# Optimization experiments

Hardware: AMD Instinct MI355X
Metric: run time of the kernel (lower is better)

The kernel has to match this reference:

```python
import jax, jax.numpy as jnp
import numpy as np

B, S, D1, D2, NH, DFF, K, L = 16, 512, 512, 256, 8, 1024, 8192, 3
DK = D2 // NH
EPS_LN = 1e-5


def layer_norm(x, g, b):
    m = jnp.mean(x, axis=-1, keepdims=True)
    v = jnp.mean((x - m) ** 2, axis=-1, keepdims=True)
    return (x - m) * jax.lax.rsqrt(v + EPS_LN) * g + b


def setup_inputs() -> dict:
    key = jax.random.key(0)
    ks = jax.random.split(key, 16)
    w = lambda k, sh: (jax.random.normal(k, sh, dtype=jnp.float32) * 0.02)
    inp = {
        'x': jax.random.normal(ks[0], (B, S, D1), dtype=jnp.float32),
        'w_in': w(ks[1], (D1, D2)), 'b_in': jnp.zeros((D2,), jnp.float32),
        # per-layer stacked transformer params, leading dim = L
        'wq': w(ks[2], (L, D2, D2)), 'bq': jnp.zeros((L, D2), jnp.float32),
        'wk': w(ks[3], (L, D2, D2)), 'bk': jnp.zeros((L, D2), jnp.float32),
        'wv': w(ks[4], (L, D2, D2)), 'bv': jnp.zeros((L, D2), jnp.float32),
        'wo': w(ks[5], (L, D2, D2)), 'bo': jnp.zeros((L, D2), jnp.float32),
        'ln1_g': jnp.ones((L, D2), jnp.float32), 'ln1_b': jnp.zeros((L, D2), jnp.float32),
        'ln2_g': jnp.ones((L, D2), jnp.float32), 'ln2_b': jnp.zeros((L, D2), jnp.float32),
        'ff1_w': w(ks[6], (L, D2, DFF)), 'ff1_b': jnp.zeros((L, DFF), jnp.float32),
        'ff2_w': w(ks[7], (L, DFF, D2)), 'ff2_b': jnp.zeros((L, D2), jnp.float32),
        'pre_g': jnp.ones((D2,), jnp.float32), 'pre_b': jnp.zeros((D2,), jnp.float32),
        # codebook ~ U(-1/K, 1/K) as in torch init
        'codebook': jax.random.uniform(ks[8], (K, D2), jnp.float32, -1.0 / K, 1.0 / K),
    }
    return inp


def _encoder(x, w_in, b_in, wq, bq, wk, bk, wv, bv, wo, bo,
             ln1_g, ln1_b, ln2_g, ln2_b, ff1_w, ff1_b, ff2_w, ff2_b,
             pre_g, pre_b, codebook):
    h = x @ w_in + b_in  # [B,S,D2]
    scale = 1.0 / jnp.sqrt(jnp.float32(DK))
    for i in range(L):
        q = (h @ wq[i] + bq[i]).reshape(B, S, NH, DK)
        k = (h @ wk[i] + bk[i]).reshape(B, S, NH, DK)
        v = (h @ wv[i] + bv[i]).reshape(B, S, NH, DK)
        scores = jnp.einsum('bqhd,bkhd->bhqk', q, k) * scale
        attn = jax.nn.softmax(scores, axis=-1)  # dropout = identity (eval)
        ctx = jnp.einsum('bhqk,bkhd->bqhd', attn, v).reshape(B, S, D2)
        h = layer_norm(h + (ctx @ wo[i] + bo[i]), ln1_g[i], ln1_b[i])
        ff = jax.nn.gelu(h @ ff1_w[i] + ff1_b[i], approximate=False) @ ff2_w[i] + ff2_b[i]
        h = layer_norm(h + ff, ln2_g[i], ln2_b[i])
    h = layer_norm(h, pre_g, pre_b)

    # --- Vector quantization (L2 branch) ---
    flat = h.reshape(-1, D2)  # [N, D2], N = B*S
    dists = (jnp.sum(flat ** 2, axis=1, keepdims=True)
             + jnp.sum(codebook ** 2, axis=1)
             - 2.0 * flat @ codebook.T)  # [N, K]
    idx = jnp.argmin(dists, axis=1)  # [N]
    quant = codebook[idx].reshape(B, S, D2)  # gather == one-hot matmul
    sg = jax.lax.stop_gradient
    e_loss = jnp.mean((sg(quant) - h) ** 2)
    q_loss = jnp.mean((quant - sg(h)) ** 2)
    loss = q_loss + 0.25 * e_loss
    quant_st = h + sg(quant - h)  # straight-through
    n = jnp.float32(flat.shape[0])
    avg_probs = jnp.zeros((K,), jnp.float32).at[idx].add(1.0) / n
    perplexity = jnp.exp(-jnp.sum(avg_probs * jnp.log(avg_probs + 1e-10)))
    return quant_st, loss, perplexity, idx.reshape(B, S)


def reference(x, w_in, b_in, wq, bq, wk, bk, wv, bv, wo, bo,
              ln1_g, ln1_b, ln2_g, ln2_b, ff1_w, ff1_b, ff2_w, ff2_b,
              pre_g, pre_b, codebook):
    return _encoder(x, w_in, b_in, wq, bq, wk, bk, wv, bv, wo, bo,
                    ln1_g, ln1_b, ln2_g, ln2_b, ff1_w, ff1_b, ff2_w, ff2_b,
                    pre_g, pre_b, codebook)
```

## Files before the change

### kernel.cpp

```cpp
#include <hip/hip_runtime.h>
#include <cfloat>
#include <math.h>


#define NTOK 8192

__device__ __forceinline__ float np_pairwise256(const float* xs, int lane) {
  float r = 0.f;
  if (lane < 16) {
    const int b = lane >> 3, j = lane & 7;
    const float* p = xs + b * 128 + j;
    r = p[0];
#pragma unroll
    for (int i = 1; i < 16; i++) r += p[i * 8];
  }
  float r0 = __shfl(r, 0), r1 = __shfl(r, 1), r2 = __shfl(r, 2), r3 = __shfl(r, 3);
  float r4 = __shfl(r, 4), r5 = __shfl(r, 5), r6 = __shfl(r, 6), r7 = __shfl(r, 7);
  float s0 = ((r0 + r1) + (r2 + r3)) + ((r4 + r5) + (r6 + r7));
  float q0 = __shfl(r, 8), q1 = __shfl(r, 9), q2 = __shfl(r, 10), q3 = __shfl(r, 11);
  float q4 = __shfl(r, 12), q5 = __shfl(r, 13), q6 = __shfl(r, 14), q7 = __shfl(r, 15);
  float s1 = ((q0 + q1) + (q2 + q3)) + ((q4 + q5) + (q6 + q7));
  return s0 + s1;
}

__device__ __forceinline__ float gelu_np(float x) {
  const float SQRT2F = 1.4142135623730951f;
  float xs = x / SQRT2F;
  float e = (float)erf((double)xs);
  float t = 1.0f + e;
  return (0.5f * x) * t;
}

__device__ __forceinline__ void gemm128_core(
    const float* __restrict__ A, int lda, const float* __restrict__ Bw,
    const float* __restrict__ bias, float* __restrict__ C,
    int N, int klen, int act, int m0, int n0)
{
  __shared__ float As[16][132];
  __shared__ float Bs[16][132];
  const int tid = threadIdx.x;
  const int tx = tid & 15, ty = tid >> 4;
  const int ar = tid >> 1;
  const int ak = (tid & 1) * 8;
  const int brr = tid >> 5;
  const int bnn = (tid & 31) * 4;
  float accb[8][8] = {};
  const float* Ap = A + (m0 + ar) * lda + ak;
  const float* Bp = Bw + brr * N + n0 + bnn;

  for (int k0 = 0; k0 < klen; k0 += 16) {
    float4 a0 = *(const float4*)(Ap);
    float4 a1 = *(const float4*)(Ap + 4);
    float4 b0 = *(const float4*)(Bp);
    float4 b1 = *(const float4*)(Bp + 8 * N);
    As[ak + 0][ar] = a0.x; As[ak + 1][ar] = a0.y;
    As[ak + 2][ar] = a0.z; As[ak + 3][ar] = a0.w;
    As[ak + 4][ar] = a1.x; As[ak + 5][ar] = a1.y;
    As[ak + 6][ar] = a1.z; As[ak + 7][ar] = a1.w;
    *(float4*)&Bs[brr][bnn] = b0;
    *(float4*)&Bs[brr + 8][bnn] = b1;
    __syncthreads();
#pragma unroll
    for (int kk = 0; kk < 16; kk++) {
      float4 av0 = *(const float4*)&As[kk][ty * 8];
      float4 av1 = *(const float4*)&As[kk][ty * 8 + 4];
      float4 bv0 = *(const float4*)&Bs[kk][tx * 4];
      float4 bv1 = *(const float4*)&Bs[kk][64 + tx * 4];
      float a[8] = {av0.x, av0.y, av0.z, av0.w, av1.x, av1.y, av1.z, av1.w};
      float b[8] = {bv0.x, bv0.y, bv0.z, bv0.w, bv1.x, bv1.y, bv1.z, bv1.w};
#pragma unroll
      for (int i = 0; i < 8; i++)
#pragma unroll
        for (int j = 0; j < 8; j++) accb[i][j] = fmaf(a[i], b[j], accb[i][j]);
    }
    __syncthreads();
    Ap += 16;
    Bp += 16 * N;
  }
  float4 bbl = make_float4(0.f, 0.f, 0.f, 0.f);
  float4 bbh = make_float4(0.f, 0.f, 0.f, 0.f);
  if (bias) {
    bbl = *(const float4*)&bias[n0 + tx * 4];
    bbh = *(const float4*)&bias[n0 + 64 + tx * 4];
  }
#pragma unroll
  for (int i = 0; i < 8; i++) {
    const int m = m0 + ty * 8 + i;
    float4 lo, hi;
    lo.x = accb[i][0] + bbl.x; lo.y = accb[i][1] + bbl.y;
    lo.z = accb[i][2] + bbl.z; lo.w = accb[i][3] + bbl.w;
    hi.x = accb[i][4] + bbh.x; hi.y = accb[i][5] + bbh.y;
    hi.z = accb[i][6] + bbh.z; hi.w = accb[i][7] + bbh.w;
    if (act == 1) {
      lo.x = gelu_np(lo.x); lo.y = gelu_np(lo.y);
      lo.z = gelu_np(lo.z); lo.w = gelu_np(lo.w);
      hi.x = gelu_np(hi.x); hi.y = gelu_np(hi.y);
      hi.z = gelu_np(hi.z); hi.w = gelu_np(hi.w);
    }
    *(float4*)&C[m * N + n0 + tx * 4] = lo;
    *(float4*)&C[m * N + n0 + 64 + tx * 4] = hi;
  }
}

__global__ __launch_bounds__(256) void qkv_kernel(
    const float* __restrict__ h,
    const float* __restrict__ wq, const float* __restrict__ bq,
    const float* __restrict__ wk, const float* __restrict__ bk,
    const float* __restrict__ wv, const float* __restrict__ bv,
    float* __restrict__ Q, float* __restrict__ K, float* __restrict__ V)
{
  const int sel = blockIdx.y >> 1;
  const int n0 = (blockIdx.y & 1) * 128;
  const float* W = (sel == 0) ? wq : (sel == 1) ? wk : wv;
  const float* bb = (sel == 0) ? bq : (sel == 1) ? bk : bv;
  float* C = (sel == 0) ? Q : (sel == 1) ? K : V;
  gemm128_core(h, 256, W, bb, C, 256, 256, 0, blockIdx.x * 128, n0);
}

__global__ __launch_bounds__(256) void gemm128_kernel(
    const float* __restrict__ A, const float* __restrict__ B,
    const float* __restrict__ bias, float* __restrict__ C,
    int N, int K, int act)
{
  gemm128_core(A, K, B, bias, C, N, K, act, blockIdx.x * 128, blockIdx.y * 128);
}

__global__ __launch_bounds__(256) void gemm64_kernel(
    const float* __restrict__ A, const float* __restrict__ B,
    const float* __restrict__ bias, float* __restrict__ C,
    int M, int N, int K, int act)
{
  __shared__ float As[2][16][68];
  __shared__ float Bs[2][16][68];
  const int tid = threadIdx.x;
  const int tx = tid & 15, ty = tid >> 4;
  const int m0 = blockIdx.x * 64, n0 = blockIdx.y * 64;
  const int ar = tid >> 2;
  const int ak = (tid & 3) * 4;
  const int br = tid >> 4;
  const int bn = (tid & 15) * 4;
  const float* Ap = A + (m0 + ar) * K + ak;
  const float* Bp = B + br * N + n0 + bn;
  float acc[4][4] = {};
  float accb[4][4] = {};
  const int nk = K >> 4;

  float4 aR = *(const float4*)(Ap);
  float4 bR = *(const float4*)(Bp);
  As[0][ak + 0][ar] = aR.x; As[0][ak + 1][ar] = aR.y;
  As[0][ak + 2][ar] = aR.z; As[0][ak + 3][ar] = aR.w;
  *(float4*)&Bs[0][br][bn] = bR;

  for (int t = 0; t < nk; t++) {
    const int p = t & 1;
    __syncthreads();
    if (t + 1 < nk) {
      aR = *(const float4*)(Ap + (t + 1) * 16);
      bR = *(const float4*)(Bp + (t + 1) * 16 * N);
    }
#pragma unroll
    for (int kk = 0; kk < 16; kk++) {
      float4 av = *(const float4*)&As[p][kk][ty * 4];
      float4 bv = *(const float4*)&Bs[p][kk][tx * 4];
      float a[4] = {av.x, av.y, av.z, av.w};
      float b[4] = {bv.x, bv.y, bv.z, bv.w};
#pragma unroll
      for (int i = 0; i < 4; i++)
#pragma unroll
        for (int j = 0; j < 4; j++) accb[i][j] = fmaf(a[i], b[j], accb[i][j]);
    }
    if (((((t + 1) << 4) % 384) == 0) || (t + 1 == nk)) {
#pragma unroll
      for (int i = 0; i < 4; i++)
#pragma unroll
        for (int j = 0; j < 4; j++) { acc[i][j] += accb[i][j]; accb[i][j] = 0.f; }
    }
    if (t + 1 < nk) {
      const int q = p ^ 1;
      As[q][ak + 0][ar] = aR.x; As[q][ak + 1][ar] = aR.y;
      As[q][ak + 2][ar] = aR.z; As[q][ak + 3][ar] = aR.w;
      *(float4*)&Bs[q][br][bn] = bR;
    }
  }
  float4 bb4 = make_float4(0.f, 0.f, 0.f, 0.f);
  if (bias) bb4 = *(const float4*)&bias[n0 + tx * 4];
#pragma unroll
  for (int i = 0; i < 4; i++) {
    float4 o;
    o.x = acc[i][0] + bb4.x;
    o.y = acc[i][1] + bb4.y;
    o.z = acc[i][2] + bb4.z;
    o.w = acc[i][3] + bb4.w;
    if (act == 1) {
      o.x = gelu_np(o.x); o.y = gelu_np(o.y);
      o.z = gelu_np(o.z); o.w = gelu_np(o.w);
    }
    *(float4*)&C[(m0 + ty * 4 + i) * N + n0 + tx * 4] = o;
  }
}

__global__ __launch_bounds__(256) void attn_kernel(
    const float* __restrict__ Q, const float* __restrict__ Kb,
    const float* __restrict__ Vb, float* __restrict__ ctx)
{
  __shared__ float Qs[64][36];
  __shared__ float Ks[2][32][36];
  __shared__ float Vs[2][32][36];
  __shared__ float Ps[64][33];
  __shared__ float l_lds[64];
  const int tid = threadIdx.x;
  const int b = blockIdx.x >> 3, h = blockIdx.x & 7;
  const int q0 = blockIdx.y * 64;
  const int base = (b * 512) * 256 + h * 32;
  const float scale = 0.17677669529663687f;

  {
    int i0 = tid * 2;
    int r = i0 >> 3, c = i0 & 7;
    *(float4*)&Qs[r][c * 4] = *(const float4*)(Q + base + (q0 + r) * 256 + c * 4);
    int i1 = i0 + 1;
    r = i1 >> 3; c = i1 & 7;
    *(float4*)&Qs[r][c * 4] = *(const float4*)(Q + base + (q0 + r) * 256 + c * 4);
  }
  if (tid < 64) l_lds[tid] = 0.f;

  const int sr = tid >> 3, sc = tid & 7;
  {
    float4 k0v = *(const float4*)(Kb + base + sr * 256 + sc * 4);
    float4 v0v = *(const float4*)(Vb + base + sr * 256 + sc * 4);
    *(float4*)&Ks[0][sr][sc * 4] = k0v;
    *(float4*)&Vs[0][sr][sc * 4] = v0v;
  }

  const int tx = tid & 15, ty = tid >> 4;
  const int tx2 = tid & 7, ty2 = tid >> 3;
  float acc[2][4] = {};

  for (int kc = 0; kc < 16; kc++) {
    const int p = kc & 1;
    __syncthreads();
    float4 kst, vst;
    if (kc < 15) {
      int tok = (kc + 1) * 32 + sr;
      kst = *(const float4*)(Kb + base + tok * 256 + sc * 4);
      vst = *(const float4*)(Vb + base + tok * 256 + sc * 4);
    }
    float s0[4] = {}, s1[4] = {};
#pragma unroll
    for (int d = 0; d < 32; d += 4) {
      float4 k0 = *(const float4*)&Ks[p][tx][d];
      float4 k1 = *(const float4*)&Ks[p][tx + 16][d];
#pragma unroll
      for (int i = 0; i < 4; i++) {
        float4 qv = *(const float4*)&Qs[ty * 4 + i][d];
        s0[i] = fmaf(qv.w, k0.w, fmaf(qv.z, k0.z, fmaf(qv.y, k0.y, fmaf(qv.x, k0.x, s0[i]))));
        s1[i] = fmaf(qv.w, k1.w, fmaf(qv.z, k1.z, fmaf(qv.y, k1.y, fmaf(qv.x, k1.x, s1[i]))));
      }
    }
    if (kc < 15) {
      *(float4*)&Ks[p ^ 1][sr][sc * 4] = kst;
      *(float4*)&Vs[p ^ 1][sr][sc * 4] = vst;
    }
    float rs[4];
#pragma unroll
    for (int i = 0; i < 4; i++) {
      float p0 = expf(s0[i] * scale);
      float p1 = expf(s1[i] * scale);
      Ps[ty * 4 + i][tx] = p0;
      Ps[ty * 4 + i][tx + 16] = p1;
      rs[i] = p0 + p1;
    }
#pragma unroll
    for (int off = 1; off < 16; off <<= 1)
#pragma unroll
      for (int i = 0; i < 4; i++) rs[i] += __shfl_xor(rs[i], off);
    if (tx == 0) {
#pragma unroll
      for (int i = 0; i < 4; i++) l_lds[ty * 4 + i] += rs[i];
    }
    __syncthreads();
#pragma unroll 4
    for (int k = 0; k < 32; k++) {
      float4 vv = *(const float4*)&Vs[p][k][tx2 * 4];
      float pa = Ps[ty2 * 2][k];
      float pb = Ps[ty2 * 2 + 1][k];
      acc[0][0] = fmaf(pa, vv.x, acc[0][0]);
      acc[0][1] = fmaf(pa, vv.y, acc[0][1]);
      acc[0][2] = fmaf(pa, vv.z, acc[0][2]);
      acc[0][3] = fmaf(pa, vv.w, acc[0][3]);
      acc[1][0] = fmaf(pb, vv.x, acc[1][0]);
      acc[1][1] = fmaf(pb, vv.y, acc[1][1]);
      acc[1][2] = fmaf(pb, vv.z, acc[1][2]);
      acc[1][3] = fmaf(pb, vv.w, acc[1][3]);
    }
  }
  __syncthreads();
#pragma unroll
  for (int i = 0; i < 2; i++) {
    float inv = 1.f / l_lds[ty2 * 2 + i];
    float4 o;
    o.x = acc[i][0] * inv; o.y = acc[i][1] * inv;
    o.z = acc[i][2] * inv; o.w = acc[i][3] * inv;
    *(float4*)(ctx + base + (q0 + ty2 * 2 + i) * 256 + tx2 * 4) = o;
  }
}

__global__ __launch_bounds__(256) void ln_kernel(
    const float* __restrict__ X, const float* __restrict__ R,
    const float* __restrict__ g, const float* __restrict__ bt,
    float* __restrict__ Y, int hasR, float* __restrict__ Atok,
    int* __restrict__ counts, float* __restrict__ lossAcc)
{
  __shared__ float rows[4][256];
  const int w = threadIdx.x >> 6, lane = threadIdx.x & 63;
  float4 gv = *(const float4*)(g + lane * 4);
  float4 bv = *(const float4*)(bt + lane * 4);
  if (counts && blockIdx.x < 32) {
    int i = blockIdx.x * 256 + threadIdx.x;
    counts[i] = 0;
    if (i == 0) lossAcc[0] = 0.f;
  }
#pragma unroll 1
  for (int rr = 0; rr < 4; rr++) {
    const int row = blockIdx.x * 16 + w * 4 + rr;
    float4 xv = *(const float4*)(X + row * 256 + lane * 4);
    if (hasR) {
      float4 rv = *(const float4*)(R + row * 256 + lane * 4);
      xv.x += rv.x; xv.y += rv.y; xv.z += rv.z; xv.w += rv.w;
    }
    *(float4*)&rows[w][lane * 4] = xv;
    __syncthreads();
    float sum = np_pairwise256(rows[w], lane);
    float mean = sum * (1.0f / 256.0f);
    float dx = xv.x - mean, dy = xv.y - mean, dz = xv.z - mean, dw = xv.w - mean;
    __syncthreads();
    float4 sq; sq.x = dx * dx; sq.y = dy * dy; sq.z = dz * dz; sq.w = dw * dw;
    *(float4*)&rows[w][lane * 4] = sq;
    __syncthreads();
    float vsum = np_pairwise256(rows[w], lane);
    float var = vsum * (1.0f / 256.0f);
    float inv = 1.0f / sqrtf(var + 1e-5f);
    float4 o;
    o.x = ((dx * inv) * gv.x) + bv.x;
    o.y = ((dy * inv) * gv.y) + bv.y;
    o.z = ((dz * inv) * gv.z) + bv.z;
    o.w = ((dw * inv) * gv.w) + bv.w;
    *(float4*)(Y + row * 256 + lane * 4) = o;
    if (Atok) {
      float4 s2; s2.x = o.x * o.x; s2.y = o.y * o.y;
      s2.z = o.z * o.z; s2.w = o.w * o.w;
      __syncthreads();
      *(float4*)&rows[w][lane * 4] = s2;
      __syncthreads();
      float asum = np_pairwise256(rows[w], lane);
      if (lane == 0) Atok[row] = asum;
    }
    __syncthreads();
  }
}

__global__ __launch_bounds__(256) void vq_partial_kernel(
    const float* __restrict__ H, const float* __restrict__ CB,
    const float* __restrict__ Atok, float* __restrict__ partV,
    int* __restrict__ partI)
{
  __shared__ float As[16][132];
  __shared__ float Bs[16][132];
  const int tid = threadIdx.x;
  const int tx = tid & 15, ty = tid >> 4;
  const int m0 = blockIdx.x * 128;
  const int cg0 = blockIdx.y * 256;
  const int ar = tid >> 1;
  const int ak = (tid & 1) * 8;
  float At[8];
#pragma unroll
  for (int i = 0; i < 8; i++) At[i] = Atok[m0 + ty * 8 + i];
  float bestV[8];
  int bestI[8];
#pragma unroll
  for (int i = 0; i < 8; i++) { bestV[i] = FLT_MAX; bestI[i] = 0; }

  for (int ct = 0; ct < 2; ct++) {
    const int c0 = cg0 + ct * 128;
    float acc[8][8] = {};
    const float* Ap = H + (m0 + ar) * 256 + ak;
    const float* Bp = CB + (c0 + ar) * 256 + ak;
    for (int k0 = 0; k0 < 256; k0 += 16) {
      float4 a0 = *(const float4*)(Ap);
      float4 a1 = *(const float4*)(Ap + 4);
      float4 c0v = *(const float4*)(Bp);
      float4 c1v = *(const float4*)(Bp + 4);
      As[ak + 0][ar] = a0.x; As[ak + 1][ar] = a0.y;
      As[ak + 2][ar] = a0.z; As[ak + 3][ar] = a0.w;
      As[ak + 4][ar] = a1.x; As[ak + 5][ar] = a1.y;
      As[ak + 6][ar] = a1.z; As[ak + 7][ar] = a1.w;
      Bs[ak + 0][ar] = c0v.x; Bs[ak + 1][ar] = c0v.y;
      Bs[ak + 2][ar] = c0v.z; Bs[ak + 3][ar] = c0v.w;
      Bs[ak + 4][ar] = c1v.x; Bs[ak + 5][ar] = c1v.y;
      Bs[ak + 6][ar] = c1v.z; Bs[ak + 7][ar] = c1v.w;
      __syncthreads();
#pragma unroll
      for (int kk = 0; kk < 16; kk++) {
        float4 av0 = *(const float4*)&As[kk][ty * 8];
        float4 av1 = *(const float4*)&As[kk][ty * 8 + 4];
        float4 bv0 = *(const float4*)&Bs[kk][tx * 4];
        float4 bv1 = *(const float4*)&Bs[kk][64 + tx * 4];
        float a[8] = {av0.x, av0.y, av0.z, av0.w, av1.x, av1.y, av1.z, av1.w};
        float b[8] = {bv0.x, bv0.y, bv0.z, bv0.w, bv1.x, bv1.y, bv1.z, bv1.w};
#pragma unroll
        for (int i = 0; i < 8; i++)
#pragma unroll
          for (int j = 0; j < 8; j++) acc[i][j] = fmaf(a[i], b[j], acc[i][j]);
      }
      __syncthreads();
      Ap += 16;
      Bp += 16;
    }
#pragma unroll
    for (int i = 0; i < 8; i++) {
#pragma unroll
      for (int j = 0; j < 8; j++) {
        int code = c0 + ((j < 4) ? (tx * 4 + j) : (64 + tx * 4 + (j - 4)));
        float v = At[i] - 2.0f * acc[i][j];
        if (v < bestV[i]) { bestV[i] = v; bestI[i] = code; }
      }
    }
  }
#pragma unroll
  for (int i = 0; i < 8; i++) {
    float v = bestV[i];
    int ii = bestI[i];
#pragma unroll
    for (int off = 1; off < 16; off <<= 1) {
      float ov = __shfl_xor(v, off);
      int oi = __shfl_xor(ii, off);
      if (ov < v || (ov == v && oi < ii)) { v = ov; ii = oi; }
    }
    if (tx == 0) {
      int token = m0 + ty * 8 + i;
      partV[token * 32 + blockIdx.y] = v;
      partI[token * 32 + blockIdx.y] = ii;
    }
  }
}

__global__ __launch_bounds__(256) void vq_final_kernel(
    const float* __restrict__ partV, const int* __restrict__ partI,
    const float* __restrict__ HN, const float* __restrict__ CB,
    float* __restrict__ outQuant, float* __restrict__ outIdxF,
    int* __restrict__ idxInt, int* __restrict__ counts,
    float* __restrict__ lossAcc)
{
  const int w = threadIdx.x >> 6, lane = threadIdx.x & 63;
  const int t = blockIdx.x * 4 + w;
  float v = (lane < 32) ? partV[t * 32 + lane] : FLT_MAX;
  int i = (lane < 32) ? partI[t * 32 + lane] : 0x7fffffff;
#pragma unroll
  for (int off = 16; off; off >>= 1) {
    float ov = __shfl_xor(v, off);
    int oi = __shfl_xor(i, off);
    if (ov < v || (ov == v && oi < i)) { v = ov; i = oi; }
  }
  int idx = __shfl(i, 0);
  const float* c = CB + idx * 256;
  const float* hh = HN + t * 256;
  float4 cv = *(const float4*)(c + lane * 4);
  float4 hv = *(const float4*)(hh + lane * 4);
  *(float4*)(outQuant + t * 256 + lane * 4) = cv;
  float ex = cv.x - hv.x, ey = cv.y - hv.y, ez = cv.z - hv.z, ew = cv.w - hv.w;
  float se = ex * ex + ey * ey + ez * ez + ew * ew;
#pragma unroll
  for (int off = 32; off; off >>= 1) se += __shfl_xor(se, off);
  if (lane == 0) {
    outIdxF[t] = (float)idx;
    idxInt[t] = idx;
    atomicAdd(&counts[idx], 1);
    atomicAdd(lossAcc, se);
  }
}

__global__ __launch_bounds__(256) void vq_stats_kernel(
    const int* __restrict__ counts, const float* __restrict__ lossAcc,
    float* __restrict__ out)
{
  float ent = 0.f;
  for (int k = threadIdx.x; k < 8192; k += 256) {
    float p = (float)counts[k] * (1.0f / 8192.0f);
    ent += p * logf(p + 1e-10f);
  }
#pragma unroll
  for (int off = 32; off; off >>= 1) ent += __shfl_xor(ent, off);
  __shared__ float ws4[4];
  const int w = threadIdx.x >> 6, lane = threadIdx.x & 63;
  if (lane == 0) ws4[w] = ent;
  __syncthreads();
  if (threadIdx.x == 0) {
    float e = ws4[0] + ws4[1] + ws4[2] + ws4[3];
    out[2097152] = 1.25f * lossAcc[0] * (1.0f / 2097152.0f);
    out[2097153] = expf(-e);
  }
}

extern "C" void kernel_launch(void* const* d_in, const int* in_sizes, int n_in,
                              void* d_out, int out_size, void* d_ws, size_t ws_size,
                              hipStream_t stream) {
  const float* x = (const float*)d_in[0];
  const float* w_in = (const float*)d_in[1];
  const float* b_in = (const float*)d_in[2];
  const float* wq = (const float*)d_in[3];
  const float* bq = (const float*)d_in[4];
  const float* wk = (const float*)d_in[5];
  const float* bk = (const float*)d_in[6];
  const float* wv = (const float*)d_in[7];
  const float* bv = (const float*)d_in[8];
  const float* wo = (const float*)d_in[9];
  const float* bo = (const float*)d_in[10];
  const float* ln1g = (const float*)d_in[11];
  const float* ln1b = (const float*)d_in[12];
  const float* ln2g = (const float*)d_in[13];
  const float* ln2b = (const float*)d_in[14];
  const float* ff1w = (const float*)d_in[15];
  const float* ff1b = (const float*)d_in[16];
  const float* ff2w = (const float*)d_in[17];
  const float* ff2b = (const float*)d_in[18];
  const float* preg = (const float*)d_in[19];
  const float* preb = (const float*)d_in[20];
  const float* cb = (const float*)d_in[21];
  float* out = (float*)d_out;

  if (ws_size < (51ull << 20)) return;
  char* ws = (char*)d_ws;
  float* h = (float*)(ws + 0);
  float* Qb = (float*)(ws + (8ull << 20));
  float* Kb2 = (float*)(ws + (16ull << 20));
  float* Vb = (float*)(ws + (24ull << 20));
  float* Cx = (float*)(ws + (32ull << 20));
  float* Ob = Qb;
  float* F1 = Kb2;
  float* F2 = Qb;
  float* HN = Qb;
  char* smallbase = ws + (48ull << 20);
  float* Atok = (float*)(smallbase);
  float* partV = (float*)(smallbase + (512ull << 10));
  int* partI = (int*)(smallbase + (512ull << 10) + (1ull << 20));
  int* idxInt = (int*)(smallbase + (512ull << 10) + (2ull << 20));
  int* counts = (int*)(smallbase + (512ull << 10) + (2ull << 20) + (64ull << 10));
  float* lossAcc = (float*)(smallbase + (512ull << 10) + (2ull << 20) + (128ull << 10));

  gemm64_kernel<<<dim3(128, 4), 256, 0, stream>>>(x, w_in, b_in, h, NTOK, 256, 512, 0);

  for (int i = 0; i < 3; i++) {
    qkv_kernel<<<dim3(64, 6), 256, 0, stream>>>(
        h, wq + i * 65536, bq + i * 256, wk + i * 65536, bk + i * 256,
        wv + i * 65536, bv + i * 256, Qb, Kb2, Vb);
    attn_kernel<<<dim3(128, 8), 256, 0, stream>>>(Qb, Kb2, Vb, Cx);
    gemm64_kernel<<<dim3(128, 4), 256, 0, stream>>>(Cx, wo + i * 65536, bo + i * 256, Ob, NTOK, 256, 256, 0);
    ln_kernel<<<512, 256, 0, stream>>>(h, Ob, ln1g + i * 256, ln1b + i * 256, h, 1, nullptr, nullptr, nullptr);
    gemm128_kernel<<<dim3(64, 8), 256, 0, stream>>>(h, ff1w + i * 262144, ff1b + i * 1024, F1, 1024, 256, 1);
    gemm64_kernel<<<dim3(128, 4), 256, 0, stream>>>(F1, ff2w + i * 262144, ff2b + i * 256, F2, NTOK, 256, 1024, 0);
    ln_kernel<<<512, 256, 0, stream>>>(h, F2, ln2g + i * 256, ln2b + i * 256, h, 1, nullptr, nullptr, nullptr);
  }
  ln_kernel<<<512, 256, 0, stream>>>(h, nullptr, preg, preb, HN, 0, Atok, counts, lossAcc);

  vq_partial_kernel<<<dim3(64, 32), 256, 0, stream>>>(HN, cb, Atok, partV, partI);
  vq_final_kernel<<<2048, 256, 0, stream>>>(partV, partI, HN, cb,
                                            out, out + 2097154, idxInt, counts, lossAcc);
  vq_stats_kernel<<<1, 256, 0, stream>>>(counts, lossAcc, out);
}
```

Baseline: 1.533 ms.

## Drop attention K/V double buffering, flatten LayerNorm to one row per wave, add zero kernel

The attention kernel stops double-buffering K/V tiles. Each chunk is now loaded synchronously into a single LDS buffer, with an extra barrier before compute. The LayerNorm kernel handles one row per wave with 2048 blocks instead of looping over four rows, aiming for more parallelism. The counts and loss zeroing move into a separate small kernel. The attention change gives up load/compute overlap for less LDS use and simpler code, and the extra launch adds overhead.

```diff
diff --git a/kernel.cpp b/kernel.cpp
--- a/kernel.cpp
+++ b/kernel.cpp
@@ -204,8 +204,8 @@
     const float* __restrict__ Vb, float* __restrict__ ctx)
 {
   __shared__ float Qs[64][36];
-  __shared__ float Ks[2][32][36];
-  __shared__ float Vs[2][32][36];
+  __shared__ float Ks[32][36];
+  __shared__ float Vs[32][36];
   __shared__ float Ps[64][33];
   __shared__ float l_lds[64];
   const int tid = threadIdx.x;
@@ -224,42 +224,30 @@
   }
   if (tid < 64) l_lds[tid] = 0.f;
 
-  const int sr = tid >> 3, sc = tid & 7;
-  {
-    float4 k0v = *(const float4*)(Kb + base + sr * 256 + sc * 4);
-    float4 v0v = *(const float4*)(Vb + base + sr * 256 + sc * 4);
-    *(float4*)&Ks[0][sr][sc * 4] = k0v;
-    *(float4*)&Vs[0][sr][sc * 4] = v0v;
-  }
-
   const int tx = tid & 15, ty = tid >> 4;
   const int tx2 = tid & 7, ty2 = tid >> 3;
   float acc[2][4] = {};
 
   for (int kc = 0; kc < 16; kc++) {
-    const int p = kc & 1;
-    __syncthreads();
-    float4 kst, vst;
-    if (kc < 15) {
-      int tok = (kc + 1) * 32 + sr;
-      kst = *(const float4*)(Kb + base + tok * 256 + sc * 4);
-      vst = *(const float4*)(Vb + base + tok * 256 + sc * 4);
-    }
+    __syncthreads();
+    {
+      int r = tid >> 3, c = tid & 7;
+      int tok = kc * 32 + r;
+      *(float4*)&Ks[r][c * 4] = *(const float4*)(Kb + base + tok * 256 + c * 4);
+      *(float4*)&Vs[r][c * 4] = *(const float4*)(Vb + base + tok * 256 + c * 4);
+    }
+    __syncthreads();
     float s0[4] = {}, s1[4] = {};
 #pragma unroll
     for (int d = 0; d < 32; d += 4) {
-      float4 k0 = *(const float4*)&Ks[p][tx][d];
-      float4 k1 = *(const float4*)&Ks[p][tx + 16][d];
+      float4 k0 = *(const float4*)&Ks[tx][d];
+      float4 k1 = *(const float4*)&Ks[tx + 16][d];
 #pragma unroll
       for (int i = 0; i < 4; i++) {
         float4 qv = *(const float4*)&Qs[ty * 4 + i][d];
         s0[i] = fmaf(qv.w, k0.w, fmaf(qv.z, k0.z, fmaf(qv.y, k0.y, fmaf(qv.x, k0.x, s0[i]))));
         s1[i] = fmaf(qv.w, k1.w, fmaf(qv.z, k1.z, fmaf(qv.y, k1.y, fmaf(qv.x, k1.x, s1[i]))));
       }
-    }
-    if (kc < 15) {
-      *(float4*)&Ks[p ^ 1][sr][sc * 4] = kst;
-      *(float4*)&Vs[p ^ 1][sr][sc * 4] = vst;
     }
     float rs[4];
 #pragma unroll
@@ -281,7 +269,7 @@
     __syncthreads();
 #pragma unroll 4
     for (int k = 0; k < 32; k++) {
-      float4 vv = *(const float4*)&Vs[p][k][tx2 * 4];
+      float4 vv = *(const float4*)&Vs[k][tx2 * 4];
       float pa = Ps[ty2 * 2][k];
       float pb = Ps[ty2 * 2 + 1][k];
       acc[0][0] = fmaf(pa, vv.x, acc[0][0]);
@@ -308,54 +296,44 @@
 __global__ __launch_bounds__(256) void ln_kernel(
     const float* __restrict__ X, const float* __restrict__ R,
     const float* __restrict__ g, const float* __restrict__ bt,
-    float* __restrict__ Y, int hasR, float* __restrict__ Atok,
-    int* __restrict__ counts, float* __restrict__ lossAcc)
+    float* __restrict__ Y, int hasR, float* __restrict__ Atok)
 {
   __shared__ float rows[4][256];
   const int w = threadIdx.x >> 6, lane = threadIdx.x & 63;
+  const int row = blockIdx.x * 4 + w;
+  float4 xv = *(const float4*)(X + row * 256 + lane * 4);
+  if (hasR) {
+    float4 rv = *(const float4*)(R + row * 256 + lane * 4);
+    xv.x += rv.x; xv.y += rv.y; xv.z += rv.z; xv.w += rv.w;
+  }
+  *(float4*)&rows[w][lane * 4] = xv;
+  __syncthreads();
+  float sum = np_pairwise256(rows[w], lane);
+  float mean = sum * (1.0f / 256.0f);
+  float dx = xv.x - mean, dy = xv.y - mean, dz = xv.z - mean, dw = xv.w - mean;
+  __syncthreads();
+  float4 sq; sq.x = dx * dx; sq.y = dy * dy; sq.z = dz * dz; sq.w = dw * dw;
+  *(float4*)&rows[w][lane * 4] = sq;
+  __syncthreads();
+  float vsum = np_pairwise256(rows[w], lane);
+  float var = vsum * (1.0f / 256.0f);
+  float inv = 1.0f / sqrtf(var + 1e-5f);
   float4 gv = *(const float4*)(g + lane * 4);
   float4 bv = *(const float4*)(bt + lane * 4);
-  if (counts && blockIdx.x < 32) {
-    int i = blockIdx.x * 256 + threadIdx.x;
-    counts[i] = 0;
-    if (i == 0) lossAcc[0] = 0.f;
-  }
-#pragma unroll 1
-  for (int rr = 0; rr < 4; rr++) {
-    const int row = blockIdx.x * 16 + w * 4 + rr;
-    float4 xv = *(const float4*)(X + row * 256 + lane * 4);
-    if (hasR) {
-      float4 rv = *(const float4*)(R + row * 256 + lane * 4);
-      xv.x += rv.x; xv.y += rv.y; xv.z += rv.z; xv.w += rv.w;
-    }
-    *(float4*)&rows[w][lane * 4] = xv;
-    __syncthreads();
-    float sum = np_pairwise256(rows[w], lane);
-    float mean = sum * (1.0f / 256.0f);
-    float dx = xv.x - mean, dy = xv.y - mean, dz = xv.z - mean, dw = xv.w - mean;
-    __syncthreads();
-    float4 sq; sq.x = dx * dx; sq.y = dy * dy; sq.z = dz * dz; sq.w = dw * dw;
-    *(float4*)&rows[w][lane * 4] = sq;
-    __syncthreads();
-    float vsum = np_pairwise256(rows[w], lane);
-    float var = vsum * (1.0f / 256.0f);
-    float inv = 1.0f / sqrtf(var + 1e-5f);
-    float4 o;
-    o.x = ((dx * inv) * gv.x) + bv.x;
-    o.y = ((dy * inv) * gv.y) + bv.y;
-    o.z = ((dz * inv) * gv.z) + bv.z;
-    o.w = ((dw * inv) * gv.w) + bv.w;
-    *(float4*)(Y + row * 256 + lane * 4) = o;
-    if (Atok) {
-      float4 s2; s2.x = o.x * o.x; s2.y = o.y * o.y;
-      s2.z = o.z * o.z; s2.w = o.w * o.w;
-      __syncthreads();
-      *(float4*)&rows[w][lane * 4] = s2;
-      __syncthreads();
-      float asum = np_pairwise256(rows[w], lane);
-      if (lane == 0) Atok[row] = asum;
-    }
-    __syncthreads();
+  float4 o;
+  o.x = ((dx * inv) * gv.x) + bv.x;
+  o.y = ((dy * inv) * gv.y) + bv.y;
+  o.z = ((dz * inv) * gv.z) + bv.z;
+  o.w = ((dw * inv) * gv.w) + bv.w;
+  *(float4*)(Y + row * 256 + lane * 4) = o;
+  if (Atok) {
+    float4 s2; s2.x = o.x * o.x; s2.y = o.y * o.y;
+    s2.z = o.z * o.z; s2.w = o.w * o.w;
+    __syncthreads();
+    *(float4*)&rows[w][lane * 4] = s2;
+    __syncthreads();
+    float asum = np_pairwise256(rows[w], lane);
+    if (lane == 0) Atok[row] = asum;
   }
 }
 
@@ -499,6 +477,12 @@
     out[2097152] = 1.25f * lossAcc[0] * (1.0f / 2097152.0f);
     out[2097153] = expf(-e);
   }
+}
+
+__global__ void zero_kernel(int* __restrict__ counts, float* __restrict__ lossAcc) {
+  int i = blockIdx.x * 256 + threadIdx.x;
+  if (i < 8192) counts[i] = 0;
+  if (i == 0) lossAcc[0] = 0.f;
 }
 
 extern "C" void kernel_launch(void* const* d_in, const int* in_sizes, int n_in,
@@ -555,13 +539,14 @@
         wv + i * 65536, bv + i * 256, Qb, Kb2, Vb);
     attn_kernel<<<dim3(128, 8), 256, 0, stream>>>(Qb, Kb2, Vb, Cx);
     gemm64_kernel<<<dim3(128, 4), 256, 0, stream>>>(Cx, wo + i * 65536, bo + i * 256, Ob, NTOK, 256, 256, 0);
-    ln_kernel<<<512, 256, 0, stream>>>(h, Ob, ln1g + i * 256, ln1b + i * 256, h, 1, nullptr, nullptr, nullptr);
+    ln_kernel<<<2048, 256, 0, stream>>>(h, Ob, ln1g + i * 256, ln1b + i * 256, h, 1, nullptr);
     gemm128_kernel<<<dim3(64, 8), 256, 0, stream>>>(h, ff1w + i * 262144, ff1b + i * 1024, F1, 1024, 256, 1);
     gemm64_kernel<<<dim3(128, 4), 256, 0, stream>>>(F1, ff2w + i * 262144, ff2b + i * 256, F2, NTOK, 256, 1024, 0);
-    ln_kernel<<<512, 256, 0, stream>>>(h, F2, ln2g + i * 256, ln2b + i * 256, h, 1, nullptr, nullptr, nullptr);
-  }
-  ln_kernel<<<512, 256, 0, stream>>>(h, nullptr, preg, preb, HN, 0, Atok, counts, lossAcc);
-
+    ln_kernel<<<2048, 256, 0, stream>>>(h, F2, ln2g + i * 256, ln2b + i * 256, h, 1, nullptr);
+  }
+  ln_kernel<<<2048, 256, 0, stream>>>(h, nullptr, preg, preb, HN, 0, Atok);
+
+  zero_kernel<<<32, 256, 0, stream>>>(counts, lossAcc);
   vq_partial_kernel<<<dim3(64, 32), 256, 0, stream>>>(HN, cb, Atok, partV, partI);
   vq_final_kernel<<<2048, 256, 0, stream>>>(partV, partI, HN, cb,
                                             out, out + 2097154, idxInt, counts, lossAcc);
```

After: 1.479 ms. 3.5% less time.
